# Performance work log

Hardware: AMD Instinct MI355X
Metric: run time of the kernel (lower is better)

## Reference

```python
import jax, jax.numpy as jnp
import numpy as np

B, S, C, H = 8, 1024, 768, 8
D = C // H  # head dim = 96
MLP = 4 * C


def setup_inputs() -> dict:
    key = jax.random.key(0)
    ks = jax.random.split(key, 12)
    sc = 0.02
    return {
        "x": jax.random.normal(ks[0], (B, S, C), jnp.float32),
        "ln1_w": jnp.ones((S, C), jnp.float32),
        "ln1_b": jnp.zeros((S, C), jnp.float32),
        "ln2_w": jnp.ones((S, C), jnp.float32),
        "ln2_b": jnp.zeros((S, C), jnp.float32),
        "qkv_w": jax.random.normal(ks[1], (C, 3 * C), jnp.float32) * sc,
        "proj_w": jax.random.normal(ks[2], (C, C), jnp.float32) * sc,
        "mlp_w1": jax.random.normal(ks[3], (C, MLP), jnp.float32) * sc,
        "mlp_b1": jnp.zeros((MLP,), jnp.float32),
        "mlp_w2": jax.random.normal(ks[4], (MLP, C), jnp.float32) * sc,
        "mlp_b2": jnp.zeros((C,), jnp.float32),
    }


def _layernorm2d(x, w, b, eps=1e-5):
    # normalizes over BOTH (seq, channel) dims, per nn.LayerNorm([length, channel])
    mu = jnp.mean(x, axis=(-2, -1), keepdims=True)
    var = jnp.mean(jnp.square(x - mu), axis=(-2, -1), keepdims=True)
    return (x - mu) * jax.lax.rsqrt(var + eps) * w + b


def _attention(x, qkv_w, proj_w):
    b, s, _ = x.shape
    qkv = (x @ qkv_w).reshape(b, s, 3, H, D)
    q, k, v = qkv[:, :, 0], qkv[:, :, 1], qkv[:, :, 2]  # [b, s, h, d]
    # NOTE: original module applies NO 1/sqrt(d) scaling
    scores = jnp.einsum("bshd,bthd->bhst", q, k)
    attn = jax.nn.softmax(scores, axis=-1)
    out = jnp.einsum("bhst,bthd->bshd", attn, v).reshape(b, s, C)
    return out @ proj_w


def reference(x, ln1_w, ln1_b, ln2_w, ln2_b, qkv_w, proj_w, mlp_w1, mlp_b1, mlp_w2, mlp_b2):
    # dropout is identity in eval mode
    h = x + _attention(_layernorm2d(x, ln1_w, ln1_b), qkv_w, proj_w)
    y = _layernorm2d(h, ln2_w, ln2_b)
    y = jax.nn.gelu(y @ mlp_w1 + mlp_b1, approximate=False)
    return h + (y @ mlp_w2 + mlp_b2)
```

## Files before the change

kernel.cpp:

```cpp
#include <hip/hip_runtime.h>
#include <hip/hip_bf16.h>

#define S_LEN 1024
#define NB 8
#define NC 768
#define NH 8
#define HD 96
#define NMLP 3072
#define SC (S_LEN*NC)
#define BS (NB*S_LEN)

typedef __attribute__((ext_vector_type(8))) unsigned short u16x8;
typedef __attribute__((ext_vector_type(4))) unsigned short u16x4;
typedef __attribute__((ext_vector_type(8))) __bf16 bf16x8;
typedef __attribute__((ext_vector_type(4))) float f32x4;

__device__ __forceinline__ unsigned short f2b(float f) {
  union { __hip_bfloat16 h; unsigned short u; } cvt;
  cvt.h = __float2bfloat16(f);
  return cvt.u;
}

__device__ __forceinline__ void gload16(const unsigned short* g, unsigned short* l) {
  __builtin_amdgcn_global_load_lds(
      (const __attribute__((address_space(1))) unsigned int*)g,
      (__attribute__((address_space(3))) unsigned int*)l, 16, 0, 0);
}

__device__ __forceinline__ float gelu_f(float v) {
  float u = v * (0.7978845608f + 0.0356774081f * v * v);
  float au = fabsf(u);
  float e = __expf(-2.0f * au);
  float th = (1.0f - e) / (1.0f + e);
  th = copysignf(th, u);
  return 0.5f * v * (1.0f + th);
}

template<int EPI>
__global__ __launch_bounds__(512, 1)
void gemm8(const unsigned short* __restrict__ A, int lda,
           const unsigned short* __restrict__ Bt, int ldb,
           void* __restrict__ Cv, int ldc, int K,
           const float* __restrict__ bias,
           const float* __restrict__ residual, int ldr,
           float* __restrict__ lnred,
           unsigned short* __restrict__ vtout)
{
  __shared__ unsigned short As[3*16384];
  __shared__ unsigned short Bs[3*8192];
  const int tid = threadIdx.x, lane = tid & 63, wid = tid >> 6;
  const int wm = wid & 3, wn = wid >> 2;
  const int r15 = lane & 15, g = lane >> 4;
  const int tm = blockIdx.x * 256, tn = blockIdx.y * 128;
  const int NT = K >> 6;

  const int srow = lane >> 3;
  const int scol = ((lane & 7) ^ srow) << 3;
  const unsigned short* Ag = A  + (size_t)(tm + wid*32 + srow)*lda + scol;
  const unsigned short* Bg = Bt + (size_t)(tn + wid*16 + srow)*ldb + scol;

  const int kx  = (r15 & 7) << 4;
  const int k0b = (g*16) ^ kx;
  const int k1b = (64 + g*16) ^ kx;
  char* AsB = (char*)As;
  char* BsB = (char*)Bs;
  const int arow = (wm*64 + r15) * 128;
  const int brow = (wn*64 + r15) * 128;

#define LDA8(m,ks) (*(const bf16x8*)(AsB + bufA + arow + (m)*2048 + ((ks) ? k1b : k0b)))
#define LDB8(n,ks) (*(const bf16x8*)(BsB + bufB + brow + (n)*2048 + ((ks) ? k1b : k0b)))
#define STGA(i,kk,bf) gload16(Ag + (size_t)((i)*8)*lda + (kk), As + (bf)*16384 + (wid*4 + (i))*512)
#define STGB(i,kk,bf) gload16(Bg + (size_t)((i)*8)*ldb + (kk), Bs + (bf)*8192  + (wid*2 + (i))*512)
#define MFMA16(a8,b8,c) __builtin_amdgcn_mfma_f32_16x16x32_bf16(a8, b8, c, 0, 0, 0)
#define SBAR() __builtin_amdgcn_sched_barrier(0)

  f32x4 acc[4][4];
  #pragma unroll
  for (int m = 0; m < 4; ++m)
    #pragma unroll
    for (int n = 0; n < 4; ++n)
      acc[m][n] = (f32x4){0.f, 0.f, 0.f, 0.f};

  STGA(0,0,0); STGA(1,0,0); STGA(2,0,0); STGA(3,0,0); STGB(0,0,0); STGB(1,0,0);
  STGA(0,64,1); STGA(1,64,1); STGA(2,64,1); STGA(3,64,1); STGB(0,64,1); STGB(1,64,1);
  asm volatile("s_waitcnt vmcnt(6)" ::: "memory");
  __builtin_amdgcn_s_barrier();

  int buf = 0, nbuf = 2;
  for (int t = 0; t < NT; ++t) {
    const int kk = (t + 2) << 6;
    const bool pre = (t + 2) < NT;
    const int bufA = buf * 32768;
    const int bufB = buf * 16384;
    bf16x8 a[4][2], b0[2][2], b1[2][2];

    #pragma unroll
    for (int m = 0; m < 4; ++m) { a[m][0] = LDA8(m,0); a[m][1] = LDA8(m,1); }
    #pragma unroll
    for (int n = 0; n < 2; ++n) { b0[n][0] = LDB8(n,0); b0[n][1] = LDB8(n,1); }
    if (pre) { STGA(0,kk,nbuf); STGA(1,kk,nbuf); STGB(0,kk,nbuf); }
    SBAR();
    __builtin_amdgcn_s_barrier();
    asm volatile("s_waitcnt lgkmcnt(0)" ::: "memory");
    SBAR();
    __builtin_amdgcn_s_setprio(1);
    #pragma unroll
    for (int m = 0; m < 4; ++m)
      #pragma unroll
      for (int n = 0; n < 2; ++n) {
        acc[m][n] = MFMA16(a[m][0], b0[n][0], acc[m][n]);
        acc[m][n] = MFMA16(a[m][1], b0[n][1], acc[m][n]);
      }
    __builtin_amdgcn_s_setprio(0);
    SBAR();
    __builtin_amdgcn_s_barrier();

    #pragma unroll
    for (int n = 0; n < 2; ++n) { b1[n][0] = LDB8(n+2,0); b1[n][1] = LDB8(n+2,1); }
    if (pre) { STGA(2,kk,nbuf); STGA(3,kk,nbuf); STGB(1,kk,nbuf); }
    SBAR();
    __builtin_amdgcn_s_barrier();
    asm volatile("s_waitcnt lgkmcnt(0)" ::: "memory");
    SBAR();
    __builtin_amdgcn_s_setprio(1);
    #pragma unroll
    for (int m = 0; m < 4; ++m)
      #pragma unroll
      for (int n = 0; n < 2; ++n) {
        acc[m][n+2] = MFMA16(a[m][0], b1[n][0], acc[m][n+2]);
        acc[m][n+2] = MFMA16(a[m][1], b1[n][1], acc[m][n+2]);
      }
    __builtin_amdgcn_s_setprio(0);
    SBAR();
    if (pre) asm volatile("s_waitcnt vmcnt(6)" ::: "memory");
    else     asm volatile("s_waitcnt vmcnt(0)" ::: "memory");
    __builtin_amdgcn_s_barrier();
    buf  = (buf  == 2) ? 0 : buf  + 1;
    nbuf = (nbuf == 2) ? 0 : nbuf + 1;
  }
#undef LDA8
#undef LDB8
#undef STGA
#undef STGB
#undef MFMA16
#undef SBAR

  unsigned short* Cu = (unsigned short*)Cv;
  float* Cf = (float*)Cv;
  float s1 = 0.f, s2 = 0.f;
  #pragma unroll
  for (int m = 0; m < 4; ++m) {
    #pragma unroll
    for (int n = 0; n < 4; ++n) {
      const int col = tn + wn*64 + n*16 + r15;
      float vv[4];
      #pragma unroll
      for (int r = 0; r < 4; ++r) {
        const int row = tm + wm*64 + m*16 + g*4 + r;
        float v = acc[m][n][r];
        if (EPI == 2 || EPI == 4) v += bias[col];
        if (EPI == 3 || EPI == 4) v += residual[(size_t)row*ldr + col];
        if (EPI == 2) v = gelu_f(v);
        if (EPI == 3) { s1 += v; s2 += v*v; }
        vv[r] = v;
        if (EPI == 5) continue;
        if (EPI == 0 || EPI == 2) Cu[(size_t)row*ldc + col] = f2b(v);
        else                      Cf[(size_t)row*ldc + col] = v;
      }
      if (EPI == 5) {
        const int row0 = tm + wm*64 + m*16 + g*4;
        if (col < 1536) {
          #pragma unroll
          for (int r = 0; r < 4; ++r)
            Cu[(size_t)(row0 + r)*ldc + col] = f2b(vv[r]);
        } else {
          const int vg = col - 1536;
          const int h = vg / HD, d = vg % HD;
          const int b = row0 >> 10, s = row0 & 1023;
          u16x4 pk = { f2b(vv[0]), f2b(vv[1]), f2b(vv[2]), f2b(vv[3]) };
          *(u16x4*)(vtout + ((size_t)((b*NH + h)*HD + d) << 10) + s) = pk;
        }
      }
    }
  }
  if (EPI == 3) {
    #pragma unroll
    for (int o = 32; o; o >>= 1) { s1 += __shfl_xor(s1, o); s2 += __shfl_xor(s2, o); }
    __syncthreads();
    float* red = (float*)As;
    if (lane == 0) { red[wid*2] = s1; red[wid*2+1] = s2; }
    __syncthreads();
    if (tid == 0) {
      float a1 = 0.f, a2 = 0.f;
      #pragma unroll
      for (int w = 0; w < 8; ++w) { a1 += red[w*2]; a2 += red[w*2+1]; }
      const int bidx = tm >> 10;
      atomicAdd(&lnred[bidx*2],     a1);
      atomicAdd(&lnred[bidx*2 + 1], a2);
    }
  }
}

__global__ __launch_bounds__(256, 2)
void flash_attn(const unsigned short* __restrict__ qkv,
                const unsigned short* __restrict__ vt,
                unsigned short* __restrict__ outb)
{
  __shared__ unsigned short Ks[128*96];
  __shared__ unsigned short Vs[96*128];
  __shared__ unsigned short Ps[128*128];
  const int tid = threadIdx.x, lane = tid & 63, wq = tid >> 6;
  const int r15 = lane & 15, g = lane >> 4;
  const int bh = blockIdx.y, b = bh >> 3, h = bh & 7;
  const int q0 = blockIdx.x * 128;
  const int swz = (r15 & 7) << 4;
  char* PsB = (char*)Ps;
  char* VsB = (char*)Vs;

  bf16x8 qf[2][3];
  {
    const unsigned short* qb = qkv + ((size_t)b*S_LEN + q0 + wq*32 + r15)*2304 + h*HD + g*8;
    #pragma unroll
    for (int n = 0; n < 2; ++n)
      #pragma unroll
      for (int kc = 0; kc < 3; ++kc)
        qf[n][kc] = *(const bf16x8*)(qb + (size_t)n*16*2304 + kc*32);
  }

  int krow[6], kcol[6], vrow[6], vcol[6];
  #pragma unroll
  for (int i = 0; i < 6; ++i) {
    const int c = (wq*6 + i)*64 + lane;
    krow[i] = c / 12;
    kcol[i] = (c % 12) * 8;
    const int L = c * 16;
    const int row = L >> 8, cb = L & 255;
    vrow[i] = row;
    vcol[i] = (cb ^ ((row & 7) << 4)) >> 1;
  }
  const unsigned short* kbase = qkv + (size_t)b*S_LEN*2304 + NC + h*HD;
  const unsigned short* vbase = vt + (size_t)bh*HD*S_LEN;

  f32x4 oacc[6][2];
  #pragma unroll
  for (int m = 0; m < 6; ++m) {
    oacc[m][0] = (f32x4){0.f,0.f,0.f,0.f};
    oacc[m][1] = (f32x4){0.f,0.f,0.f,0.f};
  }
  float mrun[2] = {-INFINITY, -INFINITY};
  float lrun[2] = {0.f, 0.f};

  for (int kt = 0; kt < 8; ++kt) {
    const unsigned short* ksrc = kbase + (size_t)kt*128*2304;
    const unsigned short* vsrc = vbase + kt*128;
    #pragma unroll
    for (int i = 0; i < 6; ++i) {
      gload16(ksrc + (size_t)krow[i]*2304 + kcol[i], Ks + (wq*6 + i)*512);
      gload16(vsrc + vrow[i]*1024 + vcol[i],         Vs + (wq*6 + i)*512);
    }
    __syncthreads();

    f32x4 sacc[8][2];
    #pragma unroll
    for (int m = 0; m < 8; ++m) {
      sacc[m][0] = (f32x4){0.f,0.f,0.f,0.f};
      sacc[m][1] = (f32x4){0.f,0.f,0.f,0.f};
    }
    __builtin_amdgcn_s_setprio(1);
    #pragma unroll
    for (int kc = 0; kc < 3; ++kc)
      #pragma unroll
      for (int m = 0; m < 8; ++m) {
        bf16x8 kf = *(const bf16x8*)(Ks + (m*16 + r15)*96 + kc*32 + g*8);
        sacc[m][0] = __builtin_amdgcn_mfma_f32_16x16x32_bf16(kf, qf[0][kc], sacc[m][0], 0,0,0);
        sacc[m][1] = __builtin_amdgcn_mfma_f32_16x16x32_bf16(kf, qf[1][kc], sacc[m][1], 0,0,0);
      }
    __builtin_amdgcn_s_setprio(0);

    #pragma unroll
    for (int n = 0; n < 2; ++n) {
      float pm = -INFINITY;
      #pragma unroll
      for (int m = 0; m < 8; ++m)
        #pragma unroll
        for (int r = 0; r < 4; ++r) pm = fmaxf(pm, sacc[m][n][r]);
      pm = fmaxf(pm, __shfl_xor(pm, 16));
      pm = fmaxf(pm, __shfl_xor(pm, 32));
      const float newm = fmaxf(mrun[n], pm);
      const float scale = __expf(mrun[n] - newm);
      mrun[n] = newm;
      const int qloc = wq*32 + n*16 + r15;
      float s = 0.f;
      #pragma unroll
      for (int m = 0; m < 8; ++m) {
        float e0 = __expf(sacc[m][n][0] - newm);
        float e1 = __expf(sacc[m][n][1] - newm);
        float e2 = __expf(sacc[m][n][2] - newm);
        float e3 = __expf(sacc[m][n][3] - newm);
        s += (e0 + e1) + (e2 + e3);
        u16x4 pk = { f2b(e0), f2b(e1), f2b(e2), f2b(e3) };
        *(u16x4*)(PsB + ((qloc*256 + m*32 + g*8) ^ swz)) = pk;
      }
      s += __shfl_xor(s, 16);
      s += __shfl_xor(s, 32);
      lrun[n] = lrun[n]*scale + s;
      #pragma unroll
      for (int m = 0; m < 6; ++m) oacc[m][n] *= scale;
    }

    #pragma unroll
    for (int kc = 0; kc < 4; ++kc) {
      bf16x8 pf0 = *(const bf16x8*)(PsB + (((wq*32      + r15)*256 + kc*64 + g*16) ^ swz));
      bf16x8 pf1 = *(const bf16x8*)(PsB + (((wq*32 + 16 + r15)*256 + kc*64 + g*16) ^ swz));
      __builtin_amdgcn_s_setprio(1);
      #pragma unroll
      for (int m = 0; m < 6; ++m) {
        bf16x8 vf = *(const bf16x8*)(VsB + (((m*16 + r15)*256 + kc*64 + g*16) ^ swz));
        oacc[m][0] = __builtin_amdgcn_mfma_f32_16x16x32_bf16(vf, pf0, oacc[m][0], 0,0,0);
        oacc[m][1] = __builtin_amdgcn_mfma_f32_16x16x32_bf16(vf, pf1, oacc[m][1], 0,0,0);
      }
      __builtin_amdgcn_s_setprio(0);
    }
    __syncthreads();
  }

  #pragma unroll
  for (int n = 0; n < 2; ++n) {
    const float inv = 1.0f / lrun[n];
    unsigned short* orow = outb + ((size_t)b*S_LEN + q0 + wq*32 + n*16 + r15)*NC + h*HD;
    #pragma unroll
    for (int m = 0; m < 6; ++m) {
      u16x4 pk = { f2b(oacc[m][n][0]*inv), f2b(oacc[m][n][1]*inv),
                   f2b(oacc[m][n][2]*inv), f2b(oacc[m][n][3]*inv) };
      *(u16x4*)(orow + m*16 + g*4) = pk;
    }
  }
}

__global__ void transpose_cast_all(const float* __restrict__ qkv_w,
                                   const float* __restrict__ proj_w,
                                   const float* __restrict__ w1,
                                   const float* __restrict__ w2,
                                   unsigned short* __restrict__ wqkvT,
                                   unsigned short* __restrict__ wprojT,
                                   unsigned short* __restrict__ w1T,
                                   unsigned short* __restrict__ w2T)
{
  int id = blockIdx.x;
  const float* W; unsigned short* Wt; int K, N, nx;
  if (id < 1728)      {            W = qkv_w;  Wt = wqkvT;  K = NC;   N = 3*NC;  nx = 72; }
  else if (id < 2304) { id -= 1728; W = proj_w; Wt = wprojT; K = NC;   N = NC;    nx = 24; }
  else if (id < 4608) { id -= 2304; W = w1;     Wt = w1T;    K = NC;   N = NMLP;  nx = 96; }
  else                { id -= 4608; W = w2;     Wt = w2T;    K = NMLP; N = NC;    nx = 24; }
  const int n0 = (id % nx) * 32, k0 = (id / nx) * 32;

  __shared__ float tile[32][33];
  const int tx = threadIdx.x & 31, ty = threadIdx.x >> 5;
  #pragma unroll
  for (int i = 0; i < 32; i += 8)
    tile[ty + i][tx] = W[(size_t)(k0 + ty + i)*N + n0 + tx];
  __syncthreads();
  #pragma unroll
  for (int i = 0; i < 32; i += 8)
    Wt[(size_t)(n0 + ty + i)*K + k0 + tx] = f2b(tile[tx][ty + i]);
}

__global__ void ln_sum(const float* __restrict__ X, float* __restrict__ red)
{
  const int b = blockIdx.x / 96, blk = blockIdx.x % 96;
  const float4* xb = (const float4*)(X + (size_t)b*SC);
  float s = 0.f, s2 = 0.f;
  #pragma unroll
  for (int i = 0; i < 8; ++i) {
    float4 v = xb[blk*2048 + i*256 + threadIdx.x];
    s  += v.x + v.y + v.z + v.w;
    s2 += v.x*v.x + v.y*v.y + v.z*v.z + v.w*v.w;
  }
  #pragma unroll
  for (int o = 32; o; o >>= 1) { s += __shfl_down(s, o); s2 += __shfl_down(s2, o); }
  __shared__ float r1[4], r2[4];
  const int w = threadIdx.x >> 6;
  if ((threadIdx.x & 63) == 0) { r1[w] = s; r2[w] = s2; }
  __syncthreads();
  if (threadIdx.x == 0) {
    atomicAdd(&red[b*2],     r1[0] + r1[1] + r1[2] + r1[3]);
    atomicAdd(&red[b*2 + 1], r2[0] + r2[1] + r2[2] + r2[3]);
  }
}

__global__ void ln_apply_f(const float* __restrict__ X, const float* __restrict__ W,
                           const float* __restrict__ Bv, const float* __restrict__ red,
                           unsigned short* __restrict__ out)
{
  const size_t i = ((size_t)blockIdx.x*256 + threadIdx.x) * 8;
  const int b = (int)(i / SC);
  const size_t r = i % SC;
  const float inv = 1.0f / (float)SC;
  const float mu = red[b*2] * inv;
  const float var = red[b*2 + 1] * inv - mu*mu;
  const float rs = rsqrtf(var + 1e-5f);
  float4 x0 = *(const float4*)(X + i),  x1 = *(const float4*)(X + i + 4);
  float4 w0 = *(const float4*)(W + r),  w1 = *(const float4*)(W + r + 4);
  float4 b0 = *(const float4*)(Bv + r), b1 = *(const float4*)(Bv + r + 4);
  u16x8 o;
  o[0] = f2b((x0.x - mu)*rs*w0.x + b0.x);
  o[1] = f2b((x0.y - mu)*rs*w0.y + b0.y);
  o[2] = f2b((x0.z - mu)*rs*w0.z + b0.z);
  o[3] = f2b((x0.w - mu)*rs*w0.w + b0.w);
  o[4] = f2b((x1.x - mu)*rs*w1.x + b1.x);
  o[5] = f2b((x1.y - mu)*rs*w1.y + b1.y);
  o[6] = f2b((x1.z - mu)*rs*w1.z + b1.z);
  o[7] = f2b((x1.w - mu)*rs*w1.w + b1.w);
  *(u16x8*)(out + i) = o;
}

extern "C" void kernel_launch(void* const* d_in, const int* in_sizes, int n_in,
                              void* d_out, int out_size, void* d_ws, size_t ws_size,
                              hipStream_t stream) {
  const float* x      = (const float*)d_in[0];
  const float* ln1_w  = (const float*)d_in[1];
  const float* ln1_b  = (const float*)d_in[2];
  const float* ln2_w  = (const float*)d_in[3];
  const float* ln2_b  = (const float*)d_in[4];
  const float* qkv_w  = (const float*)d_in[5];
  const float* proj_w = (const float*)d_in[6];
  const float* mlp_w1 = (const float*)d_in[7];
  const float* mlp_b1 = (const float*)d_in[8];
  const float* mlp_w2 = (const float*)d_in[9];
  const float* mlp_b2 = (const float*)d_in[10];
  float* out = (float*)d_out;

  char* ws = (char*)d_ws;
  size_t off = 0;
  auto alloc = [&](size_t b) { size_t o = off; off += (b + 255) & ~(size_t)255; return o; };
  unsigned short* wqkvT  = (unsigned short*)(ws + alloc((size_t)3*NC*NC*2));
  unsigned short* wprojT = (unsigned short*)(ws + alloc((size_t)NC*NC*2));
  unsigned short* w1T    = (unsigned short*)(ws + alloc((size_t)NMLP*NC*2));
  unsigned short* w2T    = (unsigned short*)(ws + alloc((size_t)NC*NMLP*2));
  unsigned short* lnbf   = (unsigned short*)(ws + alloc((size_t)BS*NC*2));
  const size_t qkvOff    = alloc((size_t)BS*3*NC*2);
  unsigned short* qkvbf  = (unsigned short*)(ws + qkvOff);
  unsigned short* vt     = (unsigned short*)(ws + alloc((size_t)NB*NH*HD*S_LEN*2));
  unsigned short* ybf    = (unsigned short*)(ws + qkvOff);
  float* hbuf            = (float*)(ws + alloc((size_t)BS*NC*4));
  float* lnred           = (float*)(ws + alloc((size_t)4*NB*4));
  (void)ws_size; (void)in_sizes; (void)n_in; (void)out_size;

  float* red1 = lnred;
  float* red2 = lnred + 2*NB;

  const dim3 blk(256);
  const dim3 blk512(512);

  hipMemsetAsync(lnred, 0, 4*NB*sizeof(float), stream);

  transpose_cast_all<<<dim3(6912), blk, 0, stream>>>(
      qkv_w, proj_w, mlp_w1, mlp_w2, wqkvT, wprojT, w1T, w2T);

  ln_sum<<<dim3(NB*96), blk, 0, stream>>>(x, red1);
  ln_apply_f<<<dim3(BS*NC/2048), blk, 0, stream>>>(x, ln1_w, ln1_b, red1, lnbf);

  gemm8<5><<<dim3(BS/256, 3*NC/128), blk512, 0, stream>>>(
      lnbf, NC, wqkvT, NC, qkvbf, 3*NC, NC, nullptr, nullptr, 0, nullptr, vt);

  flash_attn<<<dim3(S_LEN/128, NB*NH), blk, 0, stream>>>(qkvbf, vt, lnbf);

  gemm8<3><<<dim3(BS/256, NC/128), blk512, 0, stream>>>(
      lnbf, NC, wprojT, NC, hbuf, NC, NC, nullptr, x, NC, red2, nullptr);

  ln_apply_f<<<dim3(BS*NC/2048), blk, 0, stream>>>(hbuf, ln2_w, ln2_b, red2, lnbf);

  gemm8<2><<<dim3(BS/256, NMLP/128), blk512, 0, stream>>>(
      lnbf, NC, w1T, NC, ybf, NMLP, NC, mlp_b1, nullptr, 0, nullptr, nullptr);

  gemm8<4><<<dim3(BS/256, NC/128), blk512, 0, stream>>>(
      ybf, NMLP, w2T, NMLP, out, NC, NMLP, mlp_b2, hbuf, NC, nullptr, nullptr);
}
```

Before: 290.4 us.

## Add 256x256-tile GEMM for QKV and MLP-up, split V transpose into kernel

Adds a new GEMM kernel with 256x256 output tiles, double-buffered LDS split into two K-halves, and interleaved MFMA phases with barriers. It is used for the QKV projection and the first MLP layer to raise arithmetic intensity and halve the number of tile loads per output. Because the fused V-transpose epilogue is dropped, a separate transpose kernel now writes V^T, which adds a launch and an extra pass over V. gemm8 is trimmed to keep only the residual epilogues.

```diff
diff --git a/kernel.cpp b/kernel.cpp
--- a/kernel.cpp
+++ b/kernel.cpp
@@ -38,13 +38,166 @@
 
 template<int EPI>
 __global__ __launch_bounds__(512, 1)
+void gemm256k(const unsigned short* __restrict__ A, int lda,
+              const unsigned short* __restrict__ Bt, int ldb,
+              void* __restrict__ Cv, int ldc, int K,
+              const float* __restrict__ bias)
+{
+  __shared__ unsigned short As[2*2*8192];
+  __shared__ unsigned short Bs[2*2*8192];
+  const int tid = threadIdx.x, lane = tid & 63, wid = tid >> 6;
+  const int wm = wid & 1, wn = wid >> 1;
+  const int r15 = lane & 15, g = lane >> 4;
+  const int tm = blockIdx.x * 256, tn = blockIdx.y * 256;
+  const int NT = K >> 6;
+
+  const int slc  = (tid & 7) ^ ((tid >> 3) & 7);
+  const int srow = 2*(tid >> 3) + (slc >> 2);
+  const int skc  = (slc & 3) << 3;
+  const unsigned short* Ag0 = A  + (size_t)(tm +       srow)*lda + skc;
+  const unsigned short* Ag1 = A  + (size_t)(tm + 128 + srow)*lda + skc;
+  const unsigned short* Bg0 = Bt + (size_t)(tn +       srow)*ldb + skc;
+  const unsigned short* Bg1 = Bt + (size_t)(tn + 128 + srow)*ldb + skc;
+
+  const int prl = r15 >> 1;
+  const int rdo = prl*128 + (((((r15 & 1) << 2) | g) ^ prl) << 4);
+  char* AsB = (char*)As; char* BsB = (char*)Bs;
+
+#define STGA(h,kk,dd) { \
+    gload16(Ag0 + (kk) + (h)*32, As + (((dd)*2+(h))*8192) + wid*512); \
+    gload16(Ag1 + (kk) + (h)*32, As + (((dd)*2+(h))*8192) + 4096 + wid*512); }
+#define STGB(h,kk,dd) { \
+    gload16(Bg0 + (kk) + (h)*32, Bs + (((dd)*2+(h))*8192) + wid*512); \
+    gload16(Bg1 + (kk) + (h)*32, Bs + (((dd)*2+(h))*8192) + 4096 + wid*512); }
+#define LDA8(fm,h) (*(const bf16x8*)(AsB + ((d*2+(h))<<14) + (wm<<13) + ((fm)<<10) + rdo))
+#define LDB8(n,h)  (*(const bf16x8*)(BsB + ((d*2+(h))<<14) + ((wn>>1)<<13) + ((wn&1)<<12) + ((n)<<10) + rdo))
+#define MFMA(a8,b8,c) __builtin_amdgcn_mfma_f32_16x16x32_bf16(a8,b8,c,0,0,0)
+#define SBAR() __builtin_amdgcn_sched_barrier(0)
+
+  f32x4 acc[8][4];
+  #pragma unroll
+  for (int m = 0; m < 8; ++m)
+    #pragma unroll
+    for (int n = 0; n < 4; ++n)
+      acc[m][n] = (f32x4){0.f, 0.f, 0.f, 0.f};
+
+  STGA(0,0,0); STGB(0,0,0); STGA(1,0,0); STGB(1,0,0);
+  asm volatile("s_waitcnt vmcnt(4)" ::: "memory");
+  __builtin_amdgcn_s_barrier();
+
+  for (int t = 0; t < NT; ++t) {
+    const int d = t & 1, nd = d ^ 1;
+    const int kk = (t + 1) << 6;
+    const bool pre = (t + 1) < NT;
+    bf16x8 a[4], b[4];
+
+    #pragma unroll
+    for (int m = 0; m < 4; ++m) a[m] = LDA8(m, 0);
+    #pragma unroll
+    for (int n = 0; n < 4; ++n) b[n] = LDB8(n, 0);
+    if (pre) STGA(0, kk, nd);
+    SBAR();
+    __builtin_amdgcn_s_barrier();
+    asm volatile("s_waitcnt lgkmcnt(0)" ::: "memory");
+    SBAR();
+    __builtin_amdgcn_s_setprio(1);
+    #pragma unroll
+    for (int m = 0; m < 4; ++m)
+      #pragma unroll
+      for (int n = 0; n < 4; ++n)
+        acc[m][n] = MFMA(a[m], b[n], acc[m][n]);
+    __builtin_amdgcn_s_setprio(0);
+    SBAR();
+    __builtin_amdgcn_s_barrier();
+
+    #pragma unroll
+    for (int m = 0; m < 4; ++m) a[m] = LDA8(m + 4, 0);
+    if (pre) STGB(0, kk, nd);
+    SBAR();
+    __builtin_amdgcn_s_barrier();
+    asm volatile("s_waitcnt lgkmcnt(0)" ::: "memory");
+    SBAR();
+    __builtin_amdgcn_s_setprio(1);
+    #pragma unroll
+    for (int m = 0; m < 4; ++m)
+      #pragma unroll
+      for (int n = 0; n < 4; ++n)
+        acc[m + 4][n] = MFMA(a[m], b[n], acc[m + 4][n]);
+    __builtin_amdgcn_s_setprio(0);
+    SBAR();
+    if (pre) asm volatile("s_waitcnt vmcnt(4)" ::: "memory");
+    else     asm volatile("s_waitcnt vmcnt(0)" ::: "memory");
+    __builtin_amdgcn_s_barrier();
+
+    #pragma unroll
+    for (int m = 0; m < 4; ++m) a[m] = LDA8(m, 1);
+    #pragma unroll
+    for (int n = 0; n < 4; ++n) b[n] = LDB8(n, 1);
+    if (pre) STGA(1, kk, nd);
+    SBAR();
+    __builtin_amdgcn_s_barrier();
+    asm volatile("s_waitcnt lgkmcnt(0)" ::: "memory");
+    SBAR();
+    __builtin_amdgcn_s_setprio(1);
+    #pragma unroll
+    for (int m = 0; m < 4; ++m)
+      #pragma unroll
+      for (int n = 0; n < 4; ++n)
+        acc[m][n] = MFMA(a[m], b[n], acc[m][n]);
+    __builtin_amdgcn_s_setprio(0);
+    SBAR();
+    __builtin_amdgcn_s_barrier();
+
+    #pragma unroll
+    for (int m = 0; m < 4; ++m) a[m] = LDA8(m + 4, 1);
+    if (pre) STGB(1, kk, nd);
+    SBAR();
+    __builtin_amdgcn_s_barrier();
+    asm volatile("s_waitcnt lgkmcnt(0)" ::: "memory");
+    SBAR();
+    __builtin_amdgcn_s_setprio(1);
+    #pragma unroll
+    for (int m = 0; m < 4; ++m)
+      #pragma unroll
+      for (int n = 0; n < 4; ++n)
+        acc[m + 4][n] = MFMA(a[m], b[n], acc[m + 4][n]);
+    __builtin_amdgcn_s_setprio(0);
+    SBAR();
+    if (pre) asm volatile("s_waitcnt vmcnt(4)" ::: "memory");
+    __builtin_amdgcn_s_barrier();
+  }
+#undef STGA
+#undef STGB
+#undef LDA8
+#undef LDB8
+#undef MFMA
+#undef SBAR
+
+  unsigned short* Cu = (unsigned short*)Cv;
+  #pragma unroll
+  for (int m = 0; m < 8; ++m) {
+    #pragma unroll
+    for (int n = 0; n < 4; ++n) {
+      const int col = tn + wn*64 + n*16 + r15;
+      #pragma unroll
+      for (int r = 0; r < 4; ++r) {
+        const int row = tm + wm*128 + m*16 + g*4 + r;
+        float v = acc[m][n][r];
+        if (EPI == 2) { v += bias[col]; v = gelu_f(v); }
+        Cu[(size_t)row*ldc + col] = f2b(v);
+      }
+    }
+  }
+}
+
+template<int EPI>
+__global__ __launch_bounds__(512, 1)
 void gemm8(const unsigned short* __restrict__ A, int lda,
            const unsigned short* __restrict__ Bt, int ldb,
            void* __restrict__ Cv, int ldc, int K,
            const float* __restrict__ bias,
            const float* __restrict__ residual, int ldr,
-           float* __restrict__ lnred,
-           unsigned short* __restrict__ vtout)
+           float* __restrict__ lnred)
 {
   __shared__ unsigned short As[3*16384];
   __shared__ unsigned short Bs[3*8192];
@@ -145,7 +298,6 @@
 #undef MFMA16
 #undef SBAR
 
-  unsigned short* Cu = (unsigned short*)Cv;
   float* Cf = (float*)Cv;
   float s1 = 0.f, s2 = 0.f;
   #pragma unroll
@@ -153,33 +305,14 @@
     #pragma unroll
     for (int n = 0; n < 4; ++n) {
       const int col = tn + wn*64 + n*16 + r15;
-      float vv[4];
       #pragma unroll
       for (int r = 0; r < 4; ++r) {
         const int row = tm + wm*64 + m*16 + g*4 + r;
         float v = acc[m][n][r];
-        if (EPI == 2 || EPI == 4) v += bias[col];
-        if (EPI == 3 || EPI == 4) v += residual[(size_t)row*ldr + col];
-        if (EPI == 2) v = gelu_f(v);
+        if (EPI == 4) v += bias[col];
+        v += residual[(size_t)row*ldr + col];
         if (EPI == 3) { s1 += v; s2 += v*v; }
-        vv[r] = v;
-        if (EPI == 5) continue;
-        if (EPI == 0 || EPI == 2) Cu[(size_t)row*ldc + col] = f2b(v);
-        else                      Cf[(size_t)row*ldc + col] = v;
-      }
-      if (EPI == 5) {
-        const int row0 = tm + wm*64 + m*16 + g*4;
-        if (col < 1536) {
-          #pragma unroll
-          for (int r = 0; r < 4; ++r)
-            Cu[(size_t)(row0 + r)*ldc + col] = f2b(vv[r]);
-        } else {
-          const int vg = col - 1536;
-          const int h = vg / HD, d = vg % HD;
-          const int b = row0 >> 10, s = row0 & 1023;
-          u16x4 pk = { f2b(vv[0]), f2b(vv[1]), f2b(vv[2]), f2b(vv[3]) };
-          *(u16x4*)(vtout + ((size_t)((b*NH + h)*HD + d) << 10) + s) = pk;
-        }
+        Cf[(size_t)row*ldc + col] = v;
       }
     }
   }
@@ -363,6 +496,23 @@
   #pragma unroll
   for (int i = 0; i < 32; i += 8)
     Wt[(size_t)(n0 + ty + i)*K + k0 + tx] = f2b(tile[tx][ty + i]);
+}
+
+__global__ void transpose_v(const unsigned short* __restrict__ qkv, unsigned short* __restrict__ vt)
+{
+  __shared__ unsigned short tile[32][33];
+  const int bh = blockIdx.z, b = bh >> 3, h = bh & 7;
+  const unsigned short* v = qkv + (size_t)b*S_LEN*3*NC + 2*NC + h*HD;
+  unsigned short* o = vt + (size_t)bh*HD*S_LEN;
+  const int s0 = blockIdx.x * 32, d0 = blockIdx.y * 32;
+  const int tx = threadIdx.x & 31, ty = threadIdx.x >> 5;
+  #pragma unroll
+  for (int i = 0; i < 32; i += 8)
+    tile[ty + i][tx] = v[(size_t)(s0 + ty + i)*(3*NC) + d0 + tx];
+  __syncthreads();
+  #pragma unroll
+  for (int i = 0; i < 32; i += 8)
+    o[(size_t)(d0 + ty + i)*S_LEN + s0 + tx] = tile[tx][ty + i];
 }
 
 __global__ void ln_sum(const float* __restrict__ X, float* __restrict__ red)
@@ -460,19 +610,21 @@
   ln_sum<<<dim3(NB*96), blk, 0, stream>>>(x, red1);
   ln_apply_f<<<dim3(BS*NC/2048), blk, 0, stream>>>(x, ln1_w, ln1_b, red1, lnbf);
 
-  gemm8<5><<<dim3(BS/256, 3*NC/128), blk512, 0, stream>>>(
-      lnbf, NC, wqkvT, NC, qkvbf, 3*NC, NC, nullptr, nullptr, 0, nullptr, vt);
+  gemm256k<0><<<dim3(BS/256, 3*NC/256), blk512, 0, stream>>>(
+      lnbf, NC, wqkvT, NC, qkvbf, 3*NC, NC, nullptr);
+
+  transpose_v<<<dim3(S_LEN/32, HD/32, NB*NH), blk, 0, stream>>>(qkvbf, vt);
 
   flash_attn<<<dim3(S_LEN/128, NB*NH), blk, 0, stream>>>(qkvbf, vt, lnbf);
 
   gemm8<3><<<dim3(BS/256, NC/128), blk512, 0, stream>>>(
-      lnbf, NC, wprojT, NC, hbuf, NC, NC, nullptr, x, NC, red2, nullptr);
+      lnbf, NC, wprojT, NC, hbuf, NC, NC, nullptr, x, NC, red2);
 
   ln_apply_f<<<dim3(BS*NC/2048), blk, 0, stream>>>(hbuf, ln2_w, ln2_b, red2, lnbf);
 
-  gemm8<2><<<dim3(BS/256, NMLP/128), blk512, 0, stream>>>(
-      lnbf, NC, w1T, NC, ybf, NMLP, NC, mlp_b1, nullptr, 0, nullptr, nullptr);
+  gemm256k<2><<<dim3(BS/256, NMLP/256), blk512, 0, stream>>>(
+      lnbf, NC, w1T, NC, ybf, NMLP, NC, mlp_b1);
 
   gemm8<4><<<dim3(BS/256, NC/128), blk512, 0, stream>>>(
-      ybf, NMLP, w2T, NMLP, out, NC, NMLP, mlp_b2, hbuf, NC, nullptr, nullptr);
-}
+      ybf, NMLP, w2T, NMLP, out, NC, NMLP, mlp_b2, hbuf, NC, nullptr);
+}
```

After: 310.4 us. 1.07x slower.
